# Kernel tuning notes

Measured on AMD Instinct MI355X. Metric: run time of the kernel, lower is better.

## Reference

```python
import jax, jax.numpy as jnp
import numpy as np

N_HID = 8  # self.n_hidden


def _rnn_cell(x, h, Wih, Whh, bih, bhh):
    # torch.nn.RNNCell default: h' = tanh(x @ Wih^T + b_ih + h @ Whh^T + b_hh)
    return jnp.tanh(x @ Wih.T + bih + h @ Whh.T + bhh)


def setup_inputs() -> dict:
    key = jax.random.key(0)
    ks = jax.random.split(key, 15)

    def u(k, shape, fan_in):
        b = 1.0 / np.sqrt(fan_in)
        return jax.random.uniform(k, shape, jnp.float32, -b, b)

    L = 4                      # N_links = N/2 = 4
    D = 12 * L + 9             # 7 obs + (6L-2) j + 6 obsd + (6L-2) jd = 57
    return dict(
        x=jax.random.normal(ks[0], (1, D), jnp.float32),
        r_up_Wih=u(ks[1], (N_HID, 12), N_HID), r_up_Whh=u(ks[2], (N_HID, N_HID), N_HID),
        r_up_bih=u(ks[3], (N_HID,), N_HID), r_up_bhh=u(ks[4], (N_HID,), N_HID),
        fc1_W=u(ks[5], (N_HID, 13), 13), fc1_b=u(ks[6], (N_HID,), 13),
        fc2_W=u(ks[7], (N_HID, N_HID), N_HID), fc2_b=u(ks[8], (N_HID,), N_HID),
        r_down_Wih=u(ks[9], (N_HID, N_HID), N_HID), r_down_Whh=u(ks[10], (N_HID, N_HID), N_HID),
        r_down_bih=u(ks[11], (N_HID,), N_HID), r_down_bhh=u(ks[12], (N_HID,), N_HID),
        un_W=u(ks[13], (6, 2 * N_HID), 2 * N_HID), un_b=u(ks[14], (6,), 2 * N_HID),
    )


def reference(x, r_up_Wih, r_up_Whh, r_up_bih, r_up_bhh,
              fc1_W, fc1_b, fc2_W, fc2_b,
              r_down_Wih, r_down_Whh, r_down_bih, r_down_bhh,
              un_W, un_b):
    L = (x.shape[1] - 9) // 12          # N_links, static
    v = x[0]                            # batch is hard-coded to 1 in the torch code
    obs = v[:7]
    obsd = v[6 * L + 5: 6 * L + 11]     # x[:, 7+6L-2 : 7+6L-2+6]
    obs_cat = jnp.concatenate([obs, obsd])                      # [13]
    z2 = jnp.zeros((2,), v.dtype)
    jl = jnp.concatenate([z2, v[7: 6 * L + 5]]).reshape(L, 6)   # padded joint angles
    jdl = jnp.concatenate([z2, v[6 * L + 11:]]).reshape(L, 6)   # padded joint vels
    local = jnp.concatenate([jl, jdl], axis=1)                  # [L, 12]

    # upward recurrence: i = L-1 .. 0, record h BEFORE update
    def up(h, lc):
        h_new = _rnn_cell(lc, h, r_up_Wih, r_up_Whh, r_up_bih, r_up_bhh)
        return h_new, h
    _, h_pre = jax.lax.scan(up, jnp.zeros((N_HID,), v.dtype), local[::-1])
    h_up = h_pre[::-1]                  # h_up[i] as in the torch list

    h0 = jnp.tanh(fc2_W @ jnp.tanh(fc1_W @ obs_cat + fc1_b) + fc2_b)

    # downward recurrence: act from (h, h_up[i]) then h = r_down(h_up[i], h)
    def down(h, hu):
        act = un_W @ jnp.concatenate([h, hu]) + un_b
        h_new = _rnn_cell(hu, h, r_down_Wih, r_down_Whh, r_down_bih, r_down_bhh)
        return h_new, act
    _, acts = jax.lax.scan(down, h0, h_up)  # [L, 6]

    return acts.reshape(-1)[2:][None, :]    # [1, 6L-2]
```

## Files before the change

### kernel.cpp

```cpp
#include <hip/hip_runtime.h>
#include <math.h>

#define NH 8

__global__ __launch_bounds__(64) void recpolicy_kernel(
    const float* __restrict__ x,
    const float* __restrict__ up_Wih, const float* __restrict__ up_Whh,
    const float* __restrict__ up_bih, const float* __restrict__ up_bhh,
    const float* __restrict__ fc1_W, const float* __restrict__ fc1_b,
    const float* __restrict__ fc2_W, const float* __restrict__ fc2_b,
    const float* __restrict__ dn_Wih, const float* __restrict__ dn_Whh,
    const float* __restrict__ dn_bih, const float* __restrict__ dn_bhh,
    const float* __restrict__ un_W, const float* __restrict__ un_b,
    float* __restrict__ out)
{
    const int tid = threadIdx.x;
    __shared__ float s_local[4][12];
    __shared__ float s_obs[13];
    __shared__ float s_hup[4][NH];
    __shared__ float s_t1[NH];
    __shared__ float s_h[NH];
    __shared__ float s_acts[24];

    if (tid < 48) {
        int i = tid / 12, j = tid % 12;
        float val;
        if (j < 6) {
            int n = i * 6 + j;
            val = (n < 2) ? 0.f : x[n + 5];
        } else {
            int n = i * 6 + (j - 6);
            val = (n < 2) ? 0.f : x[n + 33];
        }
        s_local[i][j] = val;
    }
    if (tid < 13) s_obs[tid] = (tid < 7) ? x[tid] : x[22 + tid];
    if (tid < NH) s_hup[3][tid] = 0.f;
    __syncthreads();

    if (tid < NH) {
        float a = up_bih[tid] + up_bhh[tid];
        #pragma unroll
        for (int k = 0; k < 12; ++k) a += up_Wih[tid * 12 + k] * s_local[3][k];
        s_hup[2][tid] = tanhf(a);
    }
    __syncthreads();
    if (tid < NH) {
        float a = up_bih[tid] + up_bhh[tid];
        #pragma unroll
        for (int k = 0; k < 12; ++k) a += up_Wih[tid * 12 + k] * s_local[2][k];
        #pragma unroll
        for (int k = 0; k < NH; ++k) a += up_Whh[tid * NH + k] * s_hup[2][k];
        s_hup[1][tid] = tanhf(a);
    }
    __syncthreads();
    if (tid < NH) {
        float a = up_bih[tid] + up_bhh[tid];
        #pragma unroll
        for (int k = 0; k < 12; ++k) a += up_Wih[tid * 12 + k] * s_local[1][k];
        #pragma unroll
        for (int k = 0; k < NH; ++k) a += up_Whh[tid * NH + k] * s_hup[1][k];
        s_hup[0][tid] = tanhf(a);
    }
    __syncthreads();

    if (tid < NH) {
        float a = fc1_b[tid];
        #pragma unroll
        for (int k = 0; k < 13; ++k) a += fc1_W[tid * 13 + k] * s_obs[k];
        s_t1[tid] = tanhf(a);
    }
    __syncthreads();
    if (tid < NH) {
        float a = fc2_b[tid];
        #pragma unroll
        for (int k = 0; k < NH; ++k) a += fc2_W[tid * NH + k] * s_t1[k];
        s_h[tid] = tanhf(a);
    }
    __syncthreads();

    for (int i = 0; i < 4; ++i) {
        float hn = 0.f;
        if (tid < NH) {
            float a = dn_bih[tid] + dn_bhh[tid];
            #pragma unroll
            for (int k = 0; k < NH; ++k) a += dn_Wih[tid * NH + k] * s_hup[i][k];
            #pragma unroll
            for (int k = 0; k < NH; ++k) a += dn_Whh[tid * NH + k] * s_h[k];
            hn = tanhf(a);
        }
        if (tid >= 8 && tid < 14) {
            int m = tid - 8;
            float a = un_b[m];
            #pragma unroll
            for (int k = 0; k < NH; ++k) a += un_W[m * 16 + k] * s_h[k];
            #pragma unroll
            for (int k = 0; k < NH; ++k) a += un_W[m * 16 + 8 + k] * s_hup[i][k];
            s_acts[i * 6 + m] = a;
        }
        __syncthreads();
        if (tid < NH) s_h[tid] = hn;
        __syncthreads();
    }

    if (tid < 22) out[tid] = s_acts[tid + 2];
}

extern "C" void kernel_launch(void* const* d_in, const int* in_sizes, int n_in,
                              void* d_out, int out_size, void* d_ws, size_t ws_size,
                              hipStream_t stream) {
    (void)in_sizes; (void)n_in; (void)d_ws; (void)ws_size; (void)out_size;
    const float* x       = (const float*)d_in[0];
    const float* up_Wih  = (const float*)d_in[1];
    const float* up_Whh  = (const float*)d_in[2];
    const float* up_bih  = (const float*)d_in[3];
    const float* up_bhh  = (const float*)d_in[4];
    const float* fc1_W   = (const float*)d_in[5];
    const float* fc1_b   = (const float*)d_in[6];
    const float* fc2_W   = (const float*)d_in[7];
    const float* fc2_b   = (const float*)d_in[8];
    const float* dn_Wih  = (const float*)d_in[9];
    const float* dn_Whh  = (const float*)d_in[10];
    const float* dn_bih  = (const float*)d_in[11];
    const float* dn_bhh  = (const float*)d_in[12];
    const float* un_W    = (const float*)d_in[13];
    const float* un_b    = (const float*)d_in[14];
    float* out = (float*)d_out;

    recpolicy_kernel<<<1, 64, 0, stream>>>(
        x, up_Wih, up_Whh, up_bih, up_bhh,
        fc1_W, fc1_b, fc2_W, fc2_b,
        dn_Wih, dn_Whh, dn_bih, dn_bhh,
        un_W, un_b, out);
}
```

Measured before the change: 85.63 us.

## Stage all weights in LDS, overlap fc branch with up RNN, fast tanh

Loads every weight matrix and bias into shared memory once at kernel start, so the serial recurrence steps stop issuing dependent global loads. The fc1/fc2 head now runs on separate threads alongside the first up-RNN steps, which removes two barriers. The down-RNN hidden state is double-buffered to drop one barrier per step, and tanhf is replaced by an exp/rcp approximation. The risks are slightly different tanh accuracy and a larger upfront load burst.

```diff
diff --git a/kernel.cpp b/kernel.cpp
--- a/kernel.cpp
+++ b/kernel.cpp
@@ -2,6 +2,13 @@
 #include <math.h>
 
 #define NH 8
+
+__device__ __forceinline__ float ftanh(float v) {
+    float a = __builtin_fabsf(v);
+    float e = __expf(2.0f * a);
+    float r = 1.0f - 2.0f * __builtin_amdgcn_rcpf(e + 1.0f);
+    return __builtin_copysignf(r, v);
+}
 
 __global__ __launch_bounds__(64) void recpolicy_kernel(
     const float* __restrict__ x,
@@ -15,12 +22,17 @@
     float* __restrict__ out)
 {
     const int tid = threadIdx.x;
+
     __shared__ float s_local[4][12];
     __shared__ float s_obs[13];
     __shared__ float s_hup[4][NH];
     __shared__ float s_t1[NH];
-    __shared__ float s_h[NH];
+    __shared__ float s_h2[2][NH];
     __shared__ float s_acts[24];
+    __shared__ float s_upWih[NH * 12], s_upWhh[NH * NH], s_upb[NH];
+    __shared__ float s_f1W[NH * 13], s_f1b[NH], s_f2W[NH * NH], s_f2b[NH];
+    __shared__ float s_dnWih[NH * NH], s_dnWhh[NH * NH], s_dnb[NH];
+    __shared__ float s_unW[6 * 16], s_unb[6];
 
     if (tid < 48) {
         int i = tid / 12, j = tid % 12;
@@ -36,70 +48,86 @@
     }
     if (tid < 13) s_obs[tid] = (tid < 7) ? x[tid] : x[22 + tid];
     if (tid < NH) s_hup[3][tid] = 0.f;
+
+    { int i = tid;      s_upWih[i] = up_Wih[i]; }
+    { int i = tid + 64; if (i < 96) s_upWih[i] = up_Wih[i]; }
+    s_upWhh[tid] = up_Whh[tid];
+    if (tid < NH) s_upb[tid] = up_bih[tid] + up_bhh[tid];
+    { int i = tid;      s_f1W[i] = fc1_W[i]; }
+    { int i = tid + 64; if (i < 104) s_f1W[i] = fc1_W[i]; }
+    if (tid < NH) s_f1b[tid] = fc1_b[tid];
+    s_f2W[tid] = fc2_W[tid];
+    if (tid < NH) s_f2b[tid] = fc2_b[tid];
+    s_dnWih[tid] = dn_Wih[tid];
+    s_dnWhh[tid] = dn_Whh[tid];
+    if (tid < NH) s_dnb[tid] = dn_bih[tid] + dn_bhh[tid];
+    { int i = tid;      s_unW[i] = un_W[i]; }
+    { int i = tid + 64; if (i < 96) s_unW[i] = un_W[i]; }
+    if (tid < 6) s_unb[tid] = un_b[tid];
     __syncthreads();
 
     if (tid < NH) {
-        float a = up_bih[tid] + up_bhh[tid];
+        float a = s_upb[tid];
         #pragma unroll
-        for (int k = 0; k < 12; ++k) a += up_Wih[tid * 12 + k] * s_local[3][k];
-        s_hup[2][tid] = tanhf(a);
+        for (int k = 0; k < 12; ++k) a += s_upWih[tid * 12 + k] * s_local[3][k];
+        s_hup[2][tid] = ftanh(a);
     }
-    __syncthreads();
-    if (tid < NH) {
-        float a = up_bih[tid] + up_bhh[tid];
+    if (tid >= 16 && tid < 24) {
+        int m = tid - 16;
+        float a = s_f1b[m];
         #pragma unroll
-        for (int k = 0; k < 12; ++k) a += up_Wih[tid * 12 + k] * s_local[2][k];
-        #pragma unroll
-        for (int k = 0; k < NH; ++k) a += up_Whh[tid * NH + k] * s_hup[2][k];
-        s_hup[1][tid] = tanhf(a);
-    }
-    __syncthreads();
-    if (tid < NH) {
-        float a = up_bih[tid] + up_bhh[tid];
-        #pragma unroll
-        for (int k = 0; k < 12; ++k) a += up_Wih[tid * 12 + k] * s_local[1][k];
-        #pragma unroll
-        for (int k = 0; k < NH; ++k) a += up_Whh[tid * NH + k] * s_hup[1][k];
-        s_hup[0][tid] = tanhf(a);
+        for (int k = 0; k < 13; ++k) a += s_f1W[m * 13 + k] * s_obs[k];
+        s_t1[m] = ftanh(a);
     }
     __syncthreads();
 
     if (tid < NH) {
-        float a = fc1_b[tid];
+        float a = s_upb[tid];
         #pragma unroll
-        for (int k = 0; k < 13; ++k) a += fc1_W[tid * 13 + k] * s_obs[k];
-        s_t1[tid] = tanhf(a);
+        for (int k = 0; k < 12; ++k) a += s_upWih[tid * 12 + k] * s_local[2][k];
+        #pragma unroll
+        for (int k = 0; k < NH; ++k) a += s_upWhh[tid * NH + k] * s_hup[2][k];
+        s_hup[1][tid] = ftanh(a);
     }
-    __syncthreads();
-    if (tid < NH) {
-        float a = fc2_b[tid];
+    if (tid >= 16 && tid < 24) {
+        int m = tid - 16;
+        float a = s_f2b[m];
         #pragma unroll
-        for (int k = 0; k < NH; ++k) a += fc2_W[tid * NH + k] * s_t1[k];
-        s_h[tid] = tanhf(a);
+        for (int k = 0; k < NH; ++k) a += s_f2W[m * NH + k] * s_t1[k];
+        s_h2[0][m] = ftanh(a);
     }
     __syncthreads();
 
+    if (tid < NH) {
+        float a = s_upb[tid];
+        #pragma unroll
+        for (int k = 0; k < 12; ++k) a += s_upWih[tid * 12 + k] * s_local[1][k];
+        #pragma unroll
+        for (int k = 0; k < NH; ++k) a += s_upWhh[tid * NH + k] * s_hup[1][k];
+        s_hup[0][tid] = ftanh(a);
+    }
+    __syncthreads();
+
+    #pragma unroll
     for (int i = 0; i < 4; ++i) {
-        float hn = 0.f;
+        const float* hcur = s_h2[i & 1];
         if (tid < NH) {
-            float a = dn_bih[tid] + dn_bhh[tid];
+            float a = s_dnb[tid];
             #pragma unroll
-            for (int k = 0; k < NH; ++k) a += dn_Wih[tid * NH + k] * s_hup[i][k];
+            for (int k = 0; k < NH; ++k) a += s_dnWih[tid * NH + k] * s_hup[i][k];
             #pragma unroll
-            for (int k = 0; k < NH; ++k) a += dn_Whh[tid * NH + k] * s_h[k];
-            hn = tanhf(a);
+            for (int k = 0; k < NH; ++k) a += s_dnWhh[tid * NH + k] * hcur[k];
+            s_h2[(i + 1) & 1][tid] = ftanh(a);
         }
         if (tid >= 8 && tid < 14) {
             int m = tid - 8;
-            float a = un_b[m];
+            float a = s_unb[m];
             #pragma unroll
-            for (int k = 0; k < NH; ++k) a += un_W[m * 16 + k] * s_h[k];
+            for (int k = 0; k < NH; ++k) a += s_unW[m * 16 + k] * hcur[k];
             #pragma unroll
-            for (int k = 0; k < NH; ++k) a += un_W[m * 16 + 8 + k] * s_hup[i][k];
+            for (int k = 0; k < NH; ++k) a += s_unW[m * 16 + 8 + k] * s_hup[i][k];
             s_acts[i * 6 + m] = a;
         }
-        __syncthreads();
-        if (tid < NH) s_h[tid] = hn;
         __syncthreads();
     }
 
```

Result: no change. 84.87 us (-0.9%).
